# Kernel tuning notes

Measured on AMD Instinct MI355X. Metric: run time of the kernel, lower is better.

## Reference

```python
import jax, jax.numpy as jnp
import numpy as np

EPS = 1e-6
TOPK = 2
N_EXPERTS = 8


def setup_inputs() -> dict:
    key = jax.random.key(0)
    ks = jax.random.split(key, 6)
    B, S, H, I, E = 4, 2048, 2048, 1408, N_EXPERTS
    scale = 0.02
    return {
        "hidden_states": jax.random.normal(ks[0], (B, S, H), dtype=jnp.float32),
        "rms_weight": jnp.ones((H,), dtype=jnp.float32) + 0.01 * jax.random.normal(ks[1], (H,), dtype=jnp.float32),
        "router_weight": scale * jax.random.normal(ks[2], (E, H), dtype=jnp.float32),
        "w_gate": scale * jax.random.normal(ks[3], (E, I, H), dtype=jnp.float32),
        "w_up": scale * jax.random.normal(ks[4], (E, I, H), dtype=jnp.float32),
        "w_down": scale * jax.random.normal(ks[5], (E, H, I), dtype=jnp.float32),
    }


def reference(hidden_states, rms_weight, router_weight, w_gate, w_up, w_down):
    shape = hidden_states.shape
    H = shape[-1]
    x = hidden_states.reshape(-1, H).astype(jnp.float32)  # [T, H]

    # RMSNorm in fp32
    var = jnp.mean(x * x, axis=-1, keepdims=True)
    x = x * jax.lax.rsqrt(var + EPS) * rms_weight

    # Router (fp32 linear) + softmax over experts, then top-k of probs
    router_logits = x @ router_weight.T  # [T, E]
    probs = jax.nn.softmax(router_logits, axis=-1)
    topk_weight, indices = jax.lax.top_k(probs, TOPK)  # [T, k] sorted desc

    # normalize_top_k_affinities=True
    topk_weight = topk_weight / (jnp.sum(topk_weight, axis=-1, keepdims=True) + 1e-20)

    # Per-token per-expert combine weight: cw[t,e] = sum_k topk_weight[t,k] * [indices[t,k]==e]
    onehot = (indices[:, :, None] == jnp.arange(N_EXPERTS)[None, None, :])  # [T, k, E]
    cw = jnp.sum(topk_weight[:, :, None] * onehot.astype(topk_weight.dtype), axis=1)  # [T, E]

    # Dense per-expert GLU MLP, weighted accumulate (faithful to gather-MLP-scatter + einsum combine)
    out = jnp.zeros_like(x)
    for e in range(N_EXPERTS):
        g = x @ w_gate[e].T            # [T, I]
        u = x @ w_up[e].T              # [T, I]
        h = jax.nn.silu(g) * u         # GLU with silu act (scaling=1, bias=0)
        y = h @ w_down[e].T            # [T, H]
        out = out + cw[:, e:e + 1] * y

    return out.reshape(shape), router_logits.reshape(shape[:-1] + (N_EXPERTS,))
```

## Files before the change

kernel.cpp:

```cpp
#include <hip/hip_runtime.h>

#define T_TOK 8192
#define HDIM 2048
#define IDIM 1408
#define NEXP 8

#define BM 128
#define BN 128
#define BK 64
#define LDK 72

typedef short s16x8 __attribute__((ext_vector_type(8)));
typedef float f32x4 __attribute__((ext_vector_type(4)));
typedef unsigned short ushort_t;

__device__ __forceinline__ ushort_t f2bf(float f) {
  unsigned int u = __float_as_uint(f);
  unsigned int r = (u + 0x7fffu + ((u >> 16) & 1u)) >> 16;
  return (ushort_t)r;
}

__device__ __forceinline__ void gll16(const void* g, void* lds) {
  __builtin_amdgcn_global_load_lds(
      (const __attribute__((address_space(1))) unsigned int*)g,
      (__attribute__((address_space(3))) unsigned int*)lds, 16, 0, 0);
}

__global__ __launch_bounds__(256) void k_cast(const float* __restrict__ src,
                                              ushort_t* __restrict__ dst, int n8) {
  int i = blockIdx.x * blockDim.x + threadIdx.x;
  if (i < n8) {
    float4 f0 = ((const float4*)src)[(size_t)i * 2];
    float4 f1 = ((const float4*)src)[(size_t)i * 2 + 1];
    union { ushort_t us[8]; uint4 v; } p;
    p.us[0]=f2bf(f0.x); p.us[1]=f2bf(f0.y); p.us[2]=f2bf(f0.z); p.us[3]=f2bf(f0.w);
    p.us[4]=f2bf(f1.x); p.us[5]=f2bf(f1.y); p.us[6]=f2bf(f1.z); p.us[7]=f2bf(f1.w);
    ((uint4*)dst)[i] = p.v;
  }
}

__global__ __launch_bounds__(256) void k_rms_router(
    const float* __restrict__ x, const float* __restrict__ rmsw,
    const float* __restrict__ rw, ushort_t* __restrict__ xnorm,
    float* __restrict__ logits_out, int* __restrict__ counts,
    int* __restrict__ tokens, float* __restrict__ pairw)
{
  const int t = blockIdx.x;
  const int tid = threadIdx.x;
  const float* xr = x + (size_t)t * HDIM + tid * 8;
  float4 a = *(const float4*)xr;
  float4 b = *(const float4*)(xr + 4);
  float xi[8] = {a.x, a.y, a.z, a.w, b.x, b.y, b.z, b.w};
  float ss = 0.f;
  #pragma unroll
  for (int i = 0; i < 8; i++) ss += xi[i] * xi[i];
  #pragma unroll
  for (int o = 32; o > 0; o >>= 1) ss += __shfl_down(ss, o, 64);
  __shared__ float s_red[4];
  if ((tid & 63) == 0) s_red[tid >> 6] = ss;
  __syncthreads();
  float tot = s_red[0] + s_red[1] + s_red[2] + s_red[3];
  float rstd = rsqrtf(tot * (1.0f / HDIM) + 1e-6f);

  const float* wwp = rmsw + tid * 8;
  #pragma unroll
  for (int i = 0; i < 8; i++) xi[i] = xi[i] * rstd * wwp[i];

  union { ushort_t us[8]; uint4 v; } pk;
  #pragma unroll
  for (int i = 0; i < 8; i++) pk.us[i] = f2bf(xi[i]);
  *(uint4*)(xnorm + (size_t)t * HDIM + tid * 8) = pk.v;

  float lg[8];
  #pragma unroll
  for (int e = 0; e < 8; e++) {
    const float4* wr = (const float4*)(rw + e * HDIM + tid * 8);
    float4 w0 = wr[0], w1 = wr[1];
    lg[e] = xi[0]*w0.x + xi[1]*w0.y + xi[2]*w0.z + xi[3]*w0.w
          + xi[4]*w1.x + xi[5]*w1.y + xi[6]*w1.z + xi[7]*w1.w;
  }
  #pragma unroll
  for (int e = 0; e < 8; e++) {
    #pragma unroll
    for (int o = 32; o > 0; o >>= 1) lg[e] += __shfl_down(lg[e], o, 64);
  }
  __shared__ float s_lg[4][8];
  if ((tid & 63) == 0) {
    #pragma unroll
    for (int e = 0; e < 8; e++) s_lg[tid >> 6][e] = lg[e];
  }
  __syncthreads();
  __shared__ float s_fin[8];
  if (tid < 8) {
    float l = s_lg[0][tid] + s_lg[1][tid] + s_lg[2][tid] + s_lg[3][tid];
    logits_out[(size_t)t * NEXP + tid] = l;
    s_fin[tid] = l;
  }
  __syncthreads();
  if (tid == 0) {
    int i0 = 0;
    #pragma unroll
    for (int e = 1; e < 8; e++) if (s_fin[e] > s_fin[i0]) i0 = e;
    int i1 = (i0 == 0) ? 1 : 0;
    #pragma unroll
    for (int e = 0; e < 8; e++) if (e != i0 && s_fin[e] > s_fin[i1]) i1 = e;
    float p1 = __expf(s_fin[i1] - s_fin[i0]);
    float inv = 1.0f / (1.0f + p1);
    float w0 = inv, w1 = p1 * inv;
    int s0 = atomicAdd(&counts[i0], 1);
    tokens[i0 * T_TOK + s0] = t; pairw[i0 * T_TOK + s0] = w0;
    int s1 = atomicAdd(&counts[i1], 1);
    tokens[i1 * T_TOK + s1] = t; pairw[i1 * T_TOK + s1] = w1;
  }
}

__global__ void k_scan(const int* __restrict__ counts, int* __restrict__ basep) {
  if (threadIdx.x == 0) {
    int s = 0;
    for (int e = 0; e < NEXP; e++) { basep[e] = s; s += counts[e]; }
  }
}


__global__ __launch_bounds__(256, 3) void k_gateup_bf16(
    const ushort_t* __restrict__ xnorm, const ushort_t* __restrict__ wgb,
    const ushort_t* __restrict__ wub, const int* __restrict__ tokens,
    const int* __restrict__ counts, const int* __restrict__ basep,
    ushort_t* __restrict__ hbuf)
{
  const int e = blockIdx.z;
  const int cnt = counts[e];
  const int m0 = blockIdx.x * BM;
  if (m0 >= cnt) return;
  const int r0 = blockIdx.y * 64;
  const int tid = threadIdx.x;

  __shared__ ushort_t As[BM * BK];
  __shared__ ushort_t Bs[BN * BK];

  const int lane = tid & 63;
  const int w = tid >> 6;
  const int srow = lane >> 3;
  const int scol = ((lane & 7) ^ srow) * 8;

  const ushort_t* agp[4]; const ushort_t* bgp[4];
  #pragma unroll
  for (int i = 0; i < 4; i++) {
    const int rl = (w * 4 + i) * 8 + srow;
    const int slot = (m0 + rl < cnt) ? (m0 + rl) : (cnt - 1);
    const int tok = tokens[e * T_TOK + slot];
    agp[i] = xnorm + (size_t)tok * HDIM + scol;
    const int nrow = r0 + ((rl >> 5) << 4) + (rl & 15);
    const ushort_t* wsrc = ((rl >> 4) & 1) ? wub : wgb;
    bgp[i] = wsrc + ((size_t)e * IDIM + nrow) * HDIM + scol;
  }

  const int wm = (w & 1) * 64;
  const int wn = (w >> 1) * 64;
  const int fr = lane & 15;
  const int fq = lane >> 4;
  const int sx = fr & 7;

  f32x4 acc[4][4] = {};

  for (int k0 = 0; k0 < HDIM; k0 += BK) {
    #pragma unroll
    for (int i = 0; i < 4; i++) gll16(agp[i] + k0, &As[(w * 4 + i) * 512]);
    #pragma unroll
    for (int i = 0; i < 4; i++) gll16(bgp[i] + k0, &Bs[(w * 4 + i) * 512]);
    __syncthreads();
    #pragma unroll
    for (int kk = 0; kk < BK; kk += 32) {
      const int c0 = kk >> 3;
      s16x8 af[4], bf[4];
      #pragma unroll
      for (int mi = 0; mi < 4; mi++)
        af[mi] = *(const s16x8*)(&As[(wm + mi * 16 + fr) * BK + (((c0 + fq) ^ sx) << 3)]);
      #pragma unroll
      for (int ni = 0; ni < 4; ni++)
        bf[ni] = *(const s16x8*)(&Bs[(wn + ni * 16 + fr) * BK + (((c0 + fq) ^ sx) << 3)]);
      #pragma unroll
      for (int mi = 0; mi < 4; mi++) {
        #pragma unroll
        for (int ni = 0; ni < 4; ni++)
          acc[mi][ni] = __builtin_amdgcn_mfma_f32_16x16x32_bf16(af[mi], bf[ni], acc[mi][ni], 0, 0, 0);
      }
    }
    __syncthreads();
  }

  const int hb = basep[e];
  #pragma unroll
  for (int mi = 0; mi < 4; mi++) {
    #pragma unroll
    for (int reg = 0; reg < 4; reg++) {
      const int rl = wm + mi * 16 + fq * 4 + reg;
      if (m0 + rl < cnt) {
        ushort_t* hrow = hbuf + (size_t)(hb + m0 + rl) * IDIM + r0 + (wn >> 1);
        #pragma unroll
        for (int nj = 0; nj < 2; nj++) {
          float g = acc[mi][2 * nj][reg];
          float u = acc[mi][2 * nj + 1][reg];
          float hv = (g / (1.0f + __expf(-g))) * u;
          hrow[nj * 16 + fr] = f2bf(hv);
        }
      }
    }
  }
}

__global__ __launch_bounds__(256, 3) void k_down_bf16(
    const ushort_t* __restrict__ hbuf, const ushort_t* __restrict__ wdb,
    const int* __restrict__ tokens, const float* __restrict__ pairw,
    const int* __restrict__ counts, const int* __restrict__ basep,
    float* __restrict__ out)
{
  const int e = blockIdx.z;
  const int cnt = counts[e];
  const int m0 = blockIdx.x * BM;
  if (m0 >= cnt) return;
  const int n0 = blockIdx.y * BN;
  const int tid = threadIdx.x;
  const int hb = basep[e];

  __shared__ ushort_t As[BM * BK];
  __shared__ ushort_t Bs[BN * BK];

  const int lane = tid & 63;
  const int w = tid >> 6;
  const int srow = lane >> 3;
  const int scol = ((lane & 7) ^ srow) * 8;

  const ushort_t* agp[4]; const ushort_t* bgp[4];
  #pragma unroll
  for (int i = 0; i < 4; i++) {
    const int rl = (w * 4 + i) * 8 + srow;
    const int slot = (m0 + rl < cnt) ? (m0 + rl) : (cnt - 1);
    agp[i] = hbuf + (size_t)(hb + slot) * IDIM + scol;
    bgp[i] = wdb + ((size_t)e * HDIM + n0 + rl) * IDIM + scol;
  }

  const int wm = (w & 1) * 64;
  const int wn = (w >> 1) * 64;
  const int fr = lane & 15;
  const int fq = lane >> 4;
  const int sx = fr & 7;

  f32x4 acc[4][4] = {};

  for (int k0 = 0; k0 < IDIM; k0 += BK) {
    #pragma unroll
    for (int i = 0; i < 4; i++) gll16(agp[i] + k0, &As[(w * 4 + i) * 512]);
    #pragma unroll
    for (int i = 0; i < 4; i++) gll16(bgp[i] + k0, &Bs[(w * 4 + i) * 512]);
    __syncthreads();
    #pragma unroll
    for (int kk = 0; kk < BK; kk += 32) {
      const int c0 = kk >> 3;
      s16x8 af[4], bf[4];
      #pragma unroll
      for (int mi = 0; mi < 4; mi++)
        af[mi] = *(const s16x8*)(&As[(wm + mi * 16 + fr) * BK + (((c0 + fq) ^ sx) << 3)]);
      #pragma unroll
      for (int ni = 0; ni < 4; ni++)
        bf[ni] = *(const s16x8*)(&Bs[(wn + ni * 16 + fr) * BK + (((c0 + fq) ^ sx) << 3)]);
      #pragma unroll
      for (int mi = 0; mi < 4; mi++) {
        #pragma unroll
        for (int ni = 0; ni < 4; ni++)
          acc[mi][ni] = __builtin_amdgcn_mfma_f32_16x16x32_bf16(af[mi], bf[ni], acc[mi][ni], 0, 0, 0);
      }
    }
    __syncthreads();
  }

  #pragma unroll
  for (int mi = 0; mi < 4; mi++) {
    #pragma unroll
    for (int reg = 0; reg < 4; reg++) {
      const int rl = wm + mi * 16 + fq * 4 + reg;
      if (m0 + rl < cnt) {
        const int tok = tokens[e * T_TOK + m0 + rl];
        const float ww = pairw[e * T_TOK + m0 + rl];
        float* orow = out + (size_t)tok * HDIM + n0;
        #pragma unroll
        for (int ni = 0; ni < 4; ni++)
          atomicAdd(&orow[wn + ni * 16 + fr], ww * acc[mi][ni][reg]);
      }
    }
  }
}


__global__ __launch_bounds__(256, 2) void k_gateup_f32(
    const ushort_t* __restrict__ xnorm, const float* __restrict__ wg,
    const float* __restrict__ wu, const int* __restrict__ tokens,
    const int* __restrict__ counts, const int* __restrict__ basep,
    ushort_t* __restrict__ hbuf)
{
  const int e = blockIdx.z;
  const int cnt = counts[e];
  const int m0 = blockIdx.x * BM;
  if (m0 >= cnt) return;
  const int n0 = blockIdx.y * BN;
  const int tid = threadIdx.x;

  __shared__ ushort_t As[BM * LDK];
  __shared__ ushort_t Bgs[BN * LDK];
  __shared__ ushort_t Bus[BN * LDK];

  const int r = tid >> 1;
  const int col0 = (tid & 1) * 32;
  const int slot = (m0 + r < cnt) ? (m0 + r) : (cnt - 1);
  const int tok = tokens[e * T_TOK + slot];
  const ushort_t* asrc = xnorm + (size_t)tok * HDIM + col0;
  const float* gsrc = wg + ((size_t)e * IDIM + n0 + r) * HDIM + col0;
  const float* usrc = wu + ((size_t)e * IDIM + n0 + r) * HDIM + col0;

  const int lane = tid & 63;
  const int wid = tid >> 6;
  const int wm = (wid & 1) * 64;
  const int wn = (wid >> 1) * 64;
  const int fr = lane & 15;
  const int fq = lane >> 4;

  f32x4 accg[4][4] = {};
  f32x4 accu[4][4] = {};

  for (int k0 = 0; k0 < HDIM; k0 += BK) {
    #pragma unroll
    for (int i = 0; i < 4; i++) {
      uint4 v = *(const uint4*)(asrc + k0 + i * 8);
      *(uint4*)(&As[r * LDK + col0 + i * 8]) = v;
    }
    #pragma unroll
    for (int i = 0; i < 4; i++) {
      float4 f0 = *(const float4*)(gsrc + k0 + i * 8);
      float4 f1 = *(const float4*)(gsrc + k0 + i * 8 + 4);
      union { ushort_t us[8]; uint4 v; } p;
      p.us[0]=f2bf(f0.x); p.us[1]=f2bf(f0.y); p.us[2]=f2bf(f0.z); p.us[3]=f2bf(f0.w);
      p.us[4]=f2bf(f1.x); p.us[5]=f2bf(f1.y); p.us[6]=f2bf(f1.z); p.us[7]=f2bf(f1.w);
      *(uint4*)(&Bgs[r * LDK + col0 + i * 8]) = p.v;
    }
    #pragma unroll
    for (int i = 0; i < 4; i++) {
      float4 f0 = *(const float4*)(usrc + k0 + i * 8);
      float4 f1 = *(const float4*)(usrc + k0 + i * 8 + 4);
      union { ushort_t us[8]; uint4 v; } p;
      p.us[0]=f2bf(f0.x); p.us[1]=f2bf(f0.y); p.us[2]=f2bf(f0.z); p.us[3]=f2bf(f0.w);
      p.us[4]=f2bf(f1.x); p.us[5]=f2bf(f1.y); p.us[6]=f2bf(f1.z); p.us[7]=f2bf(f1.w);
      *(uint4*)(&Bus[r * LDK + col0 + i * 8]) = p.v;
    }
    __syncthreads();
    #pragma unroll
    for (int kk = 0; kk < BK; kk += 32) {
      s16x8 af[4], bg[4], bu[4];
      #pragma unroll
      for (int mi = 0; mi < 4; mi++)
        af[mi] = *(const s16x8*)(&As[(wm + mi * 16 + fr) * LDK + kk + fq * 8]);
      #pragma unroll
      for (int ni = 0; ni < 4; ni++) {
        bg[ni] = *(const s16x8*)(&Bgs[(wn + ni * 16 + fr) * LDK + kk + fq * 8]);
        bu[ni] = *(const s16x8*)(&Bus[(wn + ni * 16 + fr) * LDK + kk + fq * 8]);
      }
      #pragma unroll
      for (int mi = 0; mi < 4; mi++) {
        #pragma unroll
        for (int ni = 0; ni < 4; ni++) {
          accg[mi][ni] = __builtin_amdgcn_mfma_f32_16x16x32_bf16(af[mi], bg[ni], accg[mi][ni], 0, 0, 0);
          accu[mi][ni] = __builtin_amdgcn_mfma_f32_16x16x32_bf16(af[mi], bu[ni], accu[mi][ni], 0, 0, 0);
        }
      }
    }
    __syncthreads();
  }

  const int hb = basep[e];
  #pragma unroll
  for (int mi = 0; mi < 4; mi++) {
    #pragma unroll
    for (int reg = 0; reg < 4; reg++) {
      const int rl = wm + mi * 16 + fq * 4 + reg;
      if (m0 + rl < cnt) {
        ushort_t* hrow = hbuf + (size_t)(hb + m0 + rl) * IDIM + n0;
        #pragma unroll
        for (int ni = 0; ni < 4; ni++) {
          float g = accg[mi][ni][reg];
          float u = accu[mi][ni][reg];
          float hv = (g / (1.0f + __expf(-g))) * u;
          hrow[wn + ni * 16 + fr] = f2bf(hv);
        }
      }
    }
  }
}

__global__ __launch_bounds__(256, 2) void k_down_f32(
    const ushort_t* __restrict__ hbuf, const float* __restrict__ wd,
    const int* __restrict__ tokens, const float* __restrict__ pairw,
    const int* __restrict__ counts, const int* __restrict__ basep,
    float* __restrict__ out)
{
  const int e = blockIdx.z;
  const int cnt = counts[e];
  const int m0 = blockIdx.x * BM;
  if (m0 >= cnt) return;
  const int n0 = blockIdx.y * BN;
  const int tid = threadIdx.x;
  const int hb = basep[e];

  __shared__ ushort_t As[BM * LDK];
  __shared__ ushort_t Bs[BN * LDK];

  const int r = tid >> 1;
  const int col0 = (tid & 1) * 32;
  const int slot = (m0 + r < cnt) ? (m0 + r) : (cnt - 1);
  const ushort_t* asrc = hbuf + (size_t)(hb + slot) * IDIM + col0;
  const float* bsrc = wd + ((size_t)e * HDIM + n0 + r) * IDIM + col0;

  const int lane = tid & 63;
  const int wid = tid >> 6;
  const int wm = (wid & 1) * 64;
  const int wn = (wid >> 1) * 64;
  const int fr = lane & 15;
  const int fq = lane >> 4;

  f32x4 acc[4][4] = {};

  for (int k0 = 0; k0 < IDIM; k0 += BK) {
    #pragma unroll
    for (int i = 0; i < 4; i++) {
      uint4 v = *(const uint4*)(asrc + k0 + i * 8);
      *(uint4*)(&As[r * LDK + col0 + i * 8]) = v;
    }
    #pragma unroll
    for (int i = 0; i < 4; i++) {
      float4 f0 = *(const float4*)(bsrc + k0 + i * 8);
      float4 f1 = *(const float4*)(bsrc + k0 + i * 8 + 4);
      union { ushort_t us[8]; uint4 v; } p;
      p.us[0]=f2bf(f0.x); p.us[1]=f2bf(f0.y); p.us[2]=f2bf(f0.z); p.us[3]=f2bf(f0.w);
      p.us[4]=f2bf(f1.x); p.us[5]=f2bf(f1.y); p.us[6]=f2bf(f1.z); p.us[7]=f2bf(f1.w);
      *(uint4*)(&Bs[r * LDK + col0 + i * 8]) = p.v;
    }
    __syncthreads();
    #pragma unroll
    for (int kk = 0; kk < BK; kk += 32) {
      s16x8 af[4], bf[4];
      #pragma unroll
      for (int mi = 0; mi < 4; mi++)
        af[mi] = *(const s16x8*)(&As[(wm + mi * 16 + fr) * LDK + kk + fq * 8]);
      #pragma unroll
      for (int ni = 0; ni < 4; ni++)
        bf[ni] = *(const s16x8*)(&Bs[(wn + ni * 16 + fr) * LDK + kk + fq * 8]);
      #pragma unroll
      for (int mi = 0; mi < 4; mi++) {
        #pragma unroll
        for (int ni = 0; ni < 4; ni++)
          acc[mi][ni] = __builtin_amdgcn_mfma_f32_16x16x32_bf16(af[mi], bf[ni], acc[mi][ni], 0, 0, 0);
      }
    }
    __syncthreads();
  }

  #pragma unroll
  for (int mi = 0; mi < 4; mi++) {
    #pragma unroll
    for (int reg = 0; reg < 4; reg++) {
      const int rl = wm + mi * 16 + fq * 4 + reg;
      if (m0 + rl < cnt) {
        const int tok = tokens[e * T_TOK + m0 + rl];
        const float ww = pairw[e * T_TOK + m0 + rl];
        float* orow = out + (size_t)tok * HDIM + n0;
        #pragma unroll
        for (int ni = 0; ni < 4; ni++)
          atomicAdd(&orow[wn + ni * 16 + fr], ww * acc[mi][ni][reg]);
      }
    }
  }
}

extern "C" void kernel_launch(void* const* d_in, const int* in_sizes, int n_in,
                              void* d_out, int out_size, void* d_ws, size_t ws_size,
                              hipStream_t stream)
{
  (void)in_sizes; (void)n_in;
  const float* x    = (const float*)d_in[0];
  const float* rmsw = (const float*)d_in[1];
  const float* rw   = (const float*)d_in[2];
  const float* wg   = (const float*)d_in[3];
  const float* wu   = (const float*)d_in[4];
  const float* wd   = (const float*)d_in[5];
  float* out = (float*)d_out;
  float* logits_out = out + (size_t)T_TOK * HDIM;

  const size_t WB = (size_t)NEXP * IDIM * HDIM * 2;
  const size_t HB = (size_t)2 * T_TOK * IDIM * 2;
  const size_t XB = (size_t)T_TOK * HDIM * 2;
  const size_t BOOK = 1024 + 2 * (size_t)NEXP * T_TOK * 4;

  char* ws = (char*)d_ws;
  int* counts  = (int*)ws;
  int* basep   = (int*)(ws + 256);
  int* tokens  = (int*)(ws + 1024);
  float* pairw = (float*)(ws + 1024 + (size_t)NEXP * T_TOK * 4);

  hipMemsetAsync(d_out, 0, (size_t)out_size * sizeof(float), stream);
  hipMemsetAsync(d_ws, 0, 512, stream);

  const size_t NEED = BOOK + HB + 2 * WB + ((WB > XB) ? WB : XB) + 4096;
  const int n8 = (int)((size_t)NEXP * IDIM * HDIM / 8);

  if (ws_size >= NEED) {
    ushort_t* hbuf  = (ushort_t*)(ws + BOOK);
    ushort_t* wgb   = (ushort_t*)(ws + BOOK + HB);
    ushort_t* wub   = (ushort_t*)(ws + BOOK + HB + WB);
    ushort_t* xnorm = (ushort_t*)(ws + BOOK + HB + 2 * WB);
    ushort_t* wdb   = (ushort_t*)(ws + BOOK + HB + 2 * WB);

    k_cast<<<(n8 + 255) / 256, 256, 0, stream>>>(wg, wgb, n8);
    k_cast<<<(n8 + 255) / 256, 256, 0, stream>>>(wu, wub, n8);
    k_rms_router<<<T_TOK, 256, 0, stream>>>(x, rmsw, rw, xnorm, logits_out,
                                            counts, tokens, pairw);
    k_scan<<<1, 64, 0, stream>>>(counts, basep);
    k_gateup_bf16<<<dim3(T_TOK / BM, IDIM / 64, NEXP), 256, 0, stream>>>(
        xnorm, wgb, wub, tokens, counts, basep, hbuf);
    k_cast<<<(n8 + 255) / 256, 256, 0, stream>>>(wd, wdb, n8);
    k_down_bf16<<<dim3(T_TOK / BM, HDIM / BN, NEXP), 256, 0, stream>>>(
        hbuf, wdb, tokens, pairw, counts, basep, out);
  } else {
    ushort_t* xnorm = (ushort_t*)(ws + BOOK);
    ushort_t* hbuf  = (ushort_t*)(ws + BOOK + XB);

    k_rms_router<<<T_TOK, 256, 0, stream>>>(x, rmsw, rw, xnorm, logits_out,
                                            counts, tokens, pairw);
    k_scan<<<1, 64, 0, stream>>>(counts, basep);
    k_gateup_f32<<<dim3(T_TOK / BM, IDIM / BN, NEXP), 256, 0, stream>>>(
        xnorm, wg, wu, tokens, counts, basep, hbuf);
    k_down_f32<<<dim3(T_TOK / BM, HDIM / BN, NEXP), 256, 0, stream>>>(
        hbuf, wd, tokens, pairw, counts, basep, out);
  }
}
```

Baseline: 1.077 ms.

## Rewrite bf16 expert GEMMs as 256x256 tiles with double-buffered async LDS pipeline

The bf16 gate/up and down GEMM kernels move to 512-thread blocks computing 256x256 tiles. Global-to-LDS loads are split into k-halves, double-buffered and prefetched one to two tiles ahead, with explicit vmcnt/lgkmcnt waits, raw barriers and setprio around the MFMA bursts. The aim is to hide load latency behind matrix math and to raise arithmetic intensity per loaded byte. The costs are 64KB of LDS per block, more accumulator registers, lower occupancy, and more wasted work on partial expert tiles because M-tiles are now twice as large.

```diff
diff --git a/kernel.cpp b/kernel.cpp
--- a/kernel.cpp
+++ b/kernel.cpp
@@ -5,10 +5,8 @@
 #define IDIM 1408
 #define NEXP 8
 
-#define BM 128
-#define BN 128
-#define BK 64
 #define LDK 72
+#define BKF 64
 
 typedef short s16x8 __attribute__((ext_vector_type(8)));
 typedef float f32x4 __attribute__((ext_vector_type(4)));
@@ -122,7 +120,43 @@
 }
 
 
-__global__ __launch_bounds__(256, 3) void k_gateup_bf16(
+#define GEMM_PHASE(PAR, KH, H, READB, STAGE_STMT, TAIL_STMT)                         \
+  {                                                                                  \
+    s16x8 af[4];                                                                     \
+    _Pragma("unroll") for (int j = 0; j < 4; j++) {                                  \
+      const int r_ = wr * 128 + ((H) * 4 + j) * 16 + fr;                             \
+      af[j] = *(const s16x8*)&sA[PAR][KH][(size_t)r_ * 32 + ((fq ^ (r_ & 3)) << 3)]; \
+    }                                                                                \
+    if (READB) {                                                                     \
+      _Pragma("unroll") for (int n = 0; n < 4; n++) {                                \
+        const int r_ = wc * 64 + n * 16 + fr;                                        \
+        bfr[n] = *(const s16x8*)&sB[PAR][KH][(size_t)r_ * 32 + ((fq ^ (r_ & 3)) << 3)]; \
+      }                                                                              \
+    }                                                                                \
+    STAGE_STMT;                                                                      \
+    __builtin_amdgcn_s_barrier();                                                    \
+    asm volatile("s_waitcnt lgkmcnt(0)" ::: "memory");                               \
+    __builtin_amdgcn_sched_barrier(0);                                               \
+    __builtin_amdgcn_s_setprio(1);                                                   \
+    _Pragma("unroll") for (int j = 0; j < 4; j++)                                    \
+      _Pragma("unroll") for (int n = 0; n < 4; n++)                                  \
+        acc[(H) * 4 + j][n] = __builtin_amdgcn_mfma_f32_16x16x32_bf16(               \
+            af[j], bfr[n], acc[(H) * 4 + j][n], 0, 0, 0);                            \
+    __builtin_amdgcn_s_setprio(0);                                                   \
+    TAIL_STMT;                                                                       \
+    __builtin_amdgcn_s_barrier();                                                    \
+  }
+
+#define STAGE_A(P, KH, T) do {                                                       \
+    gll16(aB0 + (size_t)((T) * 64 + (KH) * 32), &sA[P][KH][w * 512]);                \
+    gll16(aB1 + (size_t)((T) * 64 + (KH) * 32), &sA[P][KH][4096 + w * 512]); } while (0)
+#define STAGE_B(P, KH, T) do {                                                       \
+    gll16(bB0 + (size_t)((T) * 64 + (KH) * 32), &sB[P][KH][w * 512]);                \
+    gll16(bB1 + (size_t)((T) * 64 + (KH) * 32), &sB[P][KH][4096 + w * 512]); } while (0)
+
+#define VMW8 asm volatile("s_waitcnt vmcnt(8)" ::: "memory")
+
+__global__ __launch_bounds__(512) void k_gateup_bf16(
     const ushort_t* __restrict__ xnorm, const ushort_t* __restrict__ wgb,
     const ushort_t* __restrict__ wub, const int* __restrict__ tokens,
     const int* __restrict__ counts, const int* __restrict__ basep,
@@ -130,86 +164,73 @@
 {
   const int e = blockIdx.z;
   const int cnt = counts[e];
-  const int m0 = blockIdx.x * BM;
+  const int m0 = blockIdx.x * 256;
   if (m0 >= cnt) return;
-  const int r0 = blockIdx.y * 64;
+  const int r0 = blockIdx.y * 128;
   const int tid = threadIdx.x;
-
-  __shared__ ushort_t As[BM * BK];
-  __shared__ ushort_t Bs[BN * BK];
-
   const int lane = tid & 63;
   const int w = tid >> 6;
-  const int srow = lane >> 3;
-  const int scol = ((lane & 7) ^ srow) * 8;
-
-  const ushort_t* agp[4]; const ushort_t* bgp[4];
-  #pragma unroll
-  for (int i = 0; i < 4; i++) {
-    const int rl = (w * 4 + i) * 8 + srow;
-    const int slot = (m0 + rl < cnt) ? (m0 + rl) : (cnt - 1);
-    const int tok = tokens[e * T_TOK + slot];
-    agp[i] = xnorm + (size_t)tok * HDIM + scol;
-    const int nrow = r0 + ((rl >> 5) << 4) + (rl & 15);
-    const ushort_t* wsrc = ((rl >> 4) & 1) ? wub : wgb;
-    bgp[i] = wsrc + ((size_t)e * IDIM + nrow) * HDIM + scol;
-  }
-
-  const int wm = (w & 1) * 64;
-  const int wn = (w >> 1) * 64;
-  const int fr = lane & 15;
-  const int fq = lane >> 4;
-  const int sx = fr & 7;
-
-  f32x4 acc[4][4] = {};
-
-  for (int k0 = 0; k0 < HDIM; k0 += BK) {
-    #pragma unroll
-    for (int i = 0; i < 4; i++) gll16(agp[i] + k0, &As[(w * 4 + i) * 512]);
-    #pragma unroll
-    for (int i = 0; i < 4; i++) gll16(bgp[i] + k0, &Bs[(w * 4 + i) * 512]);
-    __syncthreads();
-    #pragma unroll
-    for (int kk = 0; kk < BK; kk += 32) {
-      const int c0 = kk >> 3;
-      s16x8 af[4], bf[4];
-      #pragma unroll
-      for (int mi = 0; mi < 4; mi++)
-        af[mi] = *(const s16x8*)(&As[(wm + mi * 16 + fr) * BK + (((c0 + fq) ^ sx) << 3)]);
-      #pragma unroll
-      for (int ni = 0; ni < 4; ni++)
-        bf[ni] = *(const s16x8*)(&Bs[(wn + ni * 16 + fr) * BK + (((c0 + fq) ^ sx) << 3)]);
-      #pragma unroll
-      for (int mi = 0; mi < 4; mi++) {
-        #pragma unroll
-        for (int ni = 0; ni < 4; ni++)
-          acc[mi][ni] = __builtin_amdgcn_mfma_f32_16x16x32_bf16(af[mi], bf[ni], acc[mi][ni], 0, 0, 0);
-      }
-    }
-    __syncthreads();
+  const int wr = w >> 2, wc = w & 3;
+  const int fr = lane & 15, fq = lane >> 4;
+
+  __shared__ ushort_t sA[2][2][8192];
+  __shared__ ushort_t sB[2][2][8192];
+
+  const int srow = w * 16 + (lane >> 2);
+  const int sch  = ((lane & 3) ^ ((lane >> 2) & 3)) * 8;
+
+  const ushort_t *aB0, *aB1, *bB0, *bB1;
+  {
+    int rl = srow;
+    int slot = (m0 + rl < cnt) ? m0 + rl : cnt - 1;
+    aB0 = xnorm + (size_t)tokens[e * T_TOK + slot] * HDIM + sch;
+    int nrow = r0 + ((rl >> 5) << 4) + (rl & 15);
+    bB0 = (((rl >> 4) & 1) ? wub : wgb) + ((size_t)e * IDIM + nrow) * HDIM + sch;
+    rl = 128 + srow;
+    slot = (m0 + rl < cnt) ? m0 + rl : cnt - 1;
+    aB1 = xnorm + (size_t)tokens[e * T_TOK + slot] * HDIM + sch;
+    nrow = r0 + ((rl >> 5) << 4) + (rl & 15);
+    bB1 = (((rl >> 4) & 1) ? wub : wgb) + ((size_t)e * IDIM + nrow) * HDIM + sch;
+  }
+
+  f32x4 acc[8][4] = {};
+  const int NT = HDIM / 64;
+
+  STAGE_A(0, 0, 0); STAGE_B(0, 0, 0); STAGE_A(0, 1, 0); STAGE_B(0, 1, 0);
+  STAGE_A(1, 0, 1); STAGE_B(1, 0, 1);
+  asm volatile("s_waitcnt vmcnt(4)" ::: "memory");
+  __builtin_amdgcn_s_barrier();
+
+  for (int kt = 0; kt < NT; ++kt) {
+    const int par = kt & 1, nxt = par ^ 1;
+    s16x8 bfr[4];
+    GEMM_PHASE(par, 0, 0, 1, if (kt + 1 < NT) STAGE_A(nxt, 1, kt + 1), );
+    GEMM_PHASE(par, 0, 1, 0, if (kt + 1 < NT) STAGE_B(nxt, 1, kt + 1), VMW8);
+    GEMM_PHASE(par, 1, 0, 1, if (kt + 2 < NT) STAGE_A(par, 0, kt + 2), );
+    GEMM_PHASE(par, 1, 1, 0, if (kt + 2 < NT) STAGE_B(par, 0, kt + 2), VMW8);
   }
 
   const int hb = basep[e];
   #pragma unroll
-  for (int mi = 0; mi < 4; mi++) {
+  for (int mi = 0; mi < 8; mi++) {
     #pragma unroll
     for (int reg = 0; reg < 4; reg++) {
-      const int rl = wm + mi * 16 + fq * 4 + reg;
+      const int rl = wr * 128 + mi * 16 + fq * 4 + reg;
       if (m0 + rl < cnt) {
-        ushort_t* hrow = hbuf + (size_t)(hb + m0 + rl) * IDIM + r0 + (wn >> 1);
+        ushort_t* hrow = hbuf + (size_t)(hb + m0 + rl) * IDIM + r0;
         #pragma unroll
         for (int nj = 0; nj < 2; nj++) {
           float g = acc[mi][2 * nj][reg];
           float u = acc[mi][2 * nj + 1][reg];
           float hv = (g / (1.0f + __expf(-g))) * u;
-          hrow[nj * 16 + fr] = f2bf(hv);
+          hrow[(wc * 2 + nj) * 16 + fr] = f2bf(hv);
         }
       }
     }
   }
 }
 
-__global__ __launch_bounds__(256, 3) void k_down_bf16(
+__global__ __launch_bounds__(512) void k_down_bf16(
     const ushort_t* __restrict__ hbuf, const ushort_t* __restrict__ wdb,
     const int* __restrict__ tokens, const float* __restrict__ pairw,
     const int* __restrict__ counts, const int* __restrict__ basep,
@@ -217,75 +238,63 @@
 {
   const int e = blockIdx.z;
   const int cnt = counts[e];
-  const int m0 = blockIdx.x * BM;
+  const int m0 = blockIdx.x * 256;
   if (m0 >= cnt) return;
-  const int n0 = blockIdx.y * BN;
+  const int n0 = blockIdx.y * 256;
   const int tid = threadIdx.x;
   const int hb = basep[e];
-
-  __shared__ ushort_t As[BM * BK];
-  __shared__ ushort_t Bs[BN * BK];
-
   const int lane = tid & 63;
   const int w = tid >> 6;
-  const int srow = lane >> 3;
-  const int scol = ((lane & 7) ^ srow) * 8;
-
-  const ushort_t* agp[4]; const ushort_t* bgp[4];
-  #pragma unroll
-  for (int i = 0; i < 4; i++) {
-    const int rl = (w * 4 + i) * 8 + srow;
-    const int slot = (m0 + rl < cnt) ? (m0 + rl) : (cnt - 1);
-    agp[i] = hbuf + (size_t)(hb + slot) * IDIM + scol;
-    bgp[i] = wdb + ((size_t)e * HDIM + n0 + rl) * IDIM + scol;
-  }
-
-  const int wm = (w & 1) * 64;
-  const int wn = (w >> 1) * 64;
-  const int fr = lane & 15;
-  const int fq = lane >> 4;
-  const int sx = fr & 7;
-
-  f32x4 acc[4][4] = {};
-
-  for (int k0 = 0; k0 < IDIM; k0 += BK) {
-    #pragma unroll
-    for (int i = 0; i < 4; i++) gll16(agp[i] + k0, &As[(w * 4 + i) * 512]);
-    #pragma unroll
-    for (int i = 0; i < 4; i++) gll16(bgp[i] + k0, &Bs[(w * 4 + i) * 512]);
-    __syncthreads();
-    #pragma unroll
-    for (int kk = 0; kk < BK; kk += 32) {
-      const int c0 = kk >> 3;
-      s16x8 af[4], bf[4];
-      #pragma unroll
-      for (int mi = 0; mi < 4; mi++)
-        af[mi] = *(const s16x8*)(&As[(wm + mi * 16 + fr) * BK + (((c0 + fq) ^ sx) << 3)]);
-      #pragma unroll
-      for (int ni = 0; ni < 4; ni++)
-        bf[ni] = *(const s16x8*)(&Bs[(wn + ni * 16 + fr) * BK + (((c0 + fq) ^ sx) << 3)]);
-      #pragma unroll
-      for (int mi = 0; mi < 4; mi++) {
-        #pragma unroll
-        for (int ni = 0; ni < 4; ni++)
-          acc[mi][ni] = __builtin_amdgcn_mfma_f32_16x16x32_bf16(af[mi], bf[ni], acc[mi][ni], 0, 0, 0);
-      }
-    }
-    __syncthreads();
-  }
-
-  #pragma unroll
-  for (int mi = 0; mi < 4; mi++) {
+  const int wr = w >> 2, wc = w & 3;
+  const int fr = lane & 15, fq = lane >> 4;
+
+  __shared__ ushort_t sA[2][2][8192];
+  __shared__ ushort_t sB[2][2][8192];
+
+  const int srow = w * 16 + (lane >> 2);
+  const int sch  = ((lane & 3) ^ ((lane >> 2) & 3)) * 8;
+
+  const ushort_t *aB0, *aB1, *bB0, *bB1;
+  {
+    int rl = srow;
+    int slot = (m0 + rl < cnt) ? m0 + rl : cnt - 1;
+    aB0 = hbuf + (size_t)(hb + slot) * IDIM + sch;
+    bB0 = wdb + ((size_t)e * HDIM + n0 + rl) * IDIM + sch;
+    rl = 128 + srow;
+    slot = (m0 + rl < cnt) ? m0 + rl : cnt - 1;
+    aB1 = hbuf + (size_t)(hb + slot) * IDIM + sch;
+    bB1 = wdb + ((size_t)e * HDIM + n0 + rl) * IDIM + sch;
+  }
+
+  f32x4 acc[8][4] = {};
+  const int NT = IDIM / 64;
+
+  STAGE_A(0, 0, 0); STAGE_B(0, 0, 0); STAGE_A(0, 1, 0); STAGE_B(0, 1, 0);
+  STAGE_A(1, 0, 1); STAGE_B(1, 0, 1);
+  asm volatile("s_waitcnt vmcnt(4)" ::: "memory");
+  __builtin_amdgcn_s_barrier();
+
+  for (int kt = 0; kt < NT; ++kt) {
+    const int par = kt & 1, nxt = par ^ 1;
+    s16x8 bfr[4];
+    GEMM_PHASE(par, 0, 0, 1, if (kt + 1 < NT) STAGE_A(nxt, 1, kt + 1), );
+    GEMM_PHASE(par, 0, 1, 0, if (kt + 1 < NT) STAGE_B(nxt, 1, kt + 1), VMW8);
+    GEMM_PHASE(par, 1, 0, 1, if (kt + 2 < NT) STAGE_A(par, 0, kt + 2), );
+    GEMM_PHASE(par, 1, 1, 0, if (kt + 2 < NT) STAGE_B(par, 0, kt + 2), VMW8);
+  }
+
+  #pragma unroll
+  for (int mi = 0; mi < 8; mi++) {
     #pragma unroll
     for (int reg = 0; reg < 4; reg++) {
-      const int rl = wm + mi * 16 + fq * 4 + reg;
+      const int rl = wr * 128 + mi * 16 + fq * 4 + reg;
       if (m0 + rl < cnt) {
         const int tok = tokens[e * T_TOK + m0 + rl];
         const float ww = pairw[e * T_TOK + m0 + rl];
         float* orow = out + (size_t)tok * HDIM + n0;
         #pragma unroll
         for (int ni = 0; ni < 4; ni++)
-          atomicAdd(&orow[wn + ni * 16 + fr], ww * acc[mi][ni][reg]);
+          atomicAdd(&orow[wc * 64 + ni * 16 + fr], ww * acc[mi][ni][reg]);
       }
     }
   }
@@ -300,14 +309,14 @@
 {
   const int e = blockIdx.z;
   const int cnt = counts[e];
-  const int m0 = blockIdx.x * BM;
+  const int m0 = blockIdx.x * 128;
   if (m0 >= cnt) return;
-  const int n0 = blockIdx.y * BN;
+  const int n0 = blockIdx.y * 128;
   const int tid = threadIdx.x;
 
-  __shared__ ushort_t As[BM * LDK];
-  __shared__ ushort_t Bgs[BN * LDK];
-  __shared__ ushort_t Bus[BN * LDK];
+  __shared__ ushort_t As[128 * LDK];
+  __shared__ ushort_t Bgs[128 * LDK];
+  __shared__ ushort_t Bus[128 * LDK];
 
   const int r = tid >> 1;
   const int col0 = (tid & 1) * 32;
@@ -327,7 +336,7 @@
   f32x4 accg[4][4] = {};
   f32x4 accu[4][4] = {};
 
-  for (int k0 = 0; k0 < HDIM; k0 += BK) {
+  for (int k0 = 0; k0 < HDIM; k0 += BKF) {
     #pragma unroll
     for (int i = 0; i < 4; i++) {
       uint4 v = *(const uint4*)(asrc + k0 + i * 8);
@@ -353,7 +362,7 @@
     }
     __syncthreads();
     #pragma unroll
-    for (int kk = 0; kk < BK; kk += 32) {
+    for (int kk = 0; kk < BKF; kk += 32) {
       s16x8 af[4], bg[4], bu[4];
       #pragma unroll
       for (int mi = 0; mi < 4; mi++)
@@ -403,14 +412,14 @@
 {
   const int e = blockIdx.z;
   const int cnt = counts[e];
-  const int m0 = blockIdx.x * BM;
+  const int m0 = blockIdx.x * 128;
   if (m0 >= cnt) return;
-  const int n0 = blockIdx.y * BN;
+  const int n0 = blockIdx.y * 128;
   const int tid = threadIdx.x;
   const int hb = basep[e];
 
-  __shared__ ushort_t As[BM * LDK];
-  __shared__ ushort_t Bs[BN * LDK];
+  __shared__ ushort_t As[128 * LDK];
+  __shared__ ushort_t Bs[128 * LDK];
 
   const int r = tid >> 1;
   const int col0 = (tid & 1) * 32;
@@ -427,7 +436,7 @@
 
   f32x4 acc[4][4] = {};
 
-  for (int k0 = 0; k0 < IDIM; k0 += BK) {
+  for (int k0 = 0; k0 < IDIM; k0 += BKF) {
     #pragma unroll
     for (int i = 0; i < 4; i++) {
       uint4 v = *(const uint4*)(asrc + k0 + i * 8);
@@ -444,7 +453,7 @@
     }
     __syncthreads();
     #pragma unroll
-    for (int kk = 0; kk < BK; kk += 32) {
+    for (int kk = 0; kk < BKF; kk += 32) {
       s16x8 af[4], bf[4];
       #pragma unroll
       for (int mi = 0; mi < 4; mi++)
@@ -522,10 +531,10 @@
     k_rms_router<<<T_TOK, 256, 0, stream>>>(x, rmsw, rw, xnorm, logits_out,
                                             counts, tokens, pairw);
     k_scan<<<1, 64, 0, stream>>>(counts, basep);
-    k_gateup_bf16<<<dim3(T_TOK / BM, IDIM / 64, NEXP), 256, 0, stream>>>(
+    k_gateup_bf16<<<dim3(T_TOK / 256, (2 * IDIM) / 256, NEXP), 512, 0, stream>>>(
         xnorm, wgb, wub, tokens, counts, basep, hbuf);
     k_cast<<<(n8 + 255) / 256, 256, 0, stream>>>(wd, wdb, n8);
-    k_down_bf16<<<dim3(T_TOK / BM, HDIM / BN, NEXP), 256, 0, stream>>>(
+    k_down_bf16<<<dim3(T_TOK / 256, HDIM / 256, NEXP), 512, 0, stream>>>(
         hbuf, wdb, tokens, pairw, counts, basep, out);
   } else {
     ushort_t* xnorm = (ushort_t*)(ws + BOOK);
@@ -534,9 +543,9 @@
     k_rms_router<<<T_TOK, 256, 0, stream>>>(x, rmsw, rw, xnorm, logits_out,
                                             counts, tokens, pairw);
     k_scan<<<1, 64, 0, stream>>>(counts, basep);
-    k_gateup_f32<<<dim3(T_TOK / BM, IDIM / BN, NEXP), 256, 0, stream>>>(
+    k_gateup_f32<<<dim3(T_TOK / 128, IDIM / 128, NEXP), 256, 0, stream>>>(
         xnorm, wg, wu, tokens, counts, basep, hbuf);
-    k_down_f32<<<dim3(T_TOK / BM, HDIM / BN, NEXP), 256, 0, stream>>>(
+    k_down_f32<<<dim3(T_TOK / 128, HDIM / 128, NEXP), 256, 0, stream>>>(
         hbuf, wd, tokens, pairw, counts, basep, out);
   }
 }
```

Result: slower. 2.009 ms (+86.6%).

## Compact expert tile list, XCD-aware block remap, replace atomics with two-buffer combine

Applied to the files above, without the earlier changes.

Builds a compact list of (expert, m-tile) work items in the scan kernel so the grouped GEMMs launch only real tiles instead of a sparse 3D grid with early exits. Block IDs are remapped so that consecutive tiles land on the same XCD, which is meant to improve L2 reuse of weights. The down projection now writes plain stores into one of two output buffers chosen by top-k rank, and a combine kernel adds them, removing the memset and the float atomics. Occupancy hints are raised to 4 blocks per CU. The cost is an extra full-output read/write pass and a workspace buffer that reuses the gate/up weight region.

```diff
diff --git a/kernel.cpp b/kernel.cpp
--- a/kernel.cpp
+++ b/kernel.cpp
@@ -8,6 +8,7 @@
 #define BM 128
 #define BN 128
 #define BK 64
+#define NTILE_MAX 136
 #define LDK 72
 
 typedef short s16x8 __attribute__((ext_vector_type(8)));
@@ -24,6 +25,12 @@
   __builtin_amdgcn_global_load_lds(
       (const __attribute__((address_space(1))) unsigned int*)g,
       (__attribute__((address_space(3))) unsigned int*)lds, 16, 0, 0);
+}
+
+__device__ __forceinline__ int xcd_remap(int orig, int nwg) {
+  const int q = nwg >> 3, r = nwg & 7;
+  const int x = orig & 7, i = orig >> 3;
+  return (x < r ? x * (q + 1) : r * (q + 1) + (x - r) * q) + i;
 }
 
 __global__ __launch_bounds__(256) void k_cast(const float* __restrict__ src,
@@ -43,7 +50,8 @@
     const float* __restrict__ x, const float* __restrict__ rmsw,
     const float* __restrict__ rw, ushort_t* __restrict__ xnorm,
     float* __restrict__ logits_out, int* __restrict__ counts,
-    int* __restrict__ tokens, float* __restrict__ pairw)
+    int* __restrict__ tokens, float* __restrict__ pairw,
+    int* __restrict__ ranks)
 {
   const int t = blockIdx.x;
   const int tid = threadIdx.x;
@@ -108,31 +116,44 @@
     float inv = 1.0f / (1.0f + p1);
     float w0 = inv, w1 = p1 * inv;
     int s0 = atomicAdd(&counts[i0], 1);
-    tokens[i0 * T_TOK + s0] = t; pairw[i0 * T_TOK + s0] = w0;
+    tokens[i0 * T_TOK + s0] = t; pairw[i0 * T_TOK + s0] = w0; ranks[i0 * T_TOK + s0] = 0;
     int s1 = atomicAdd(&counts[i1], 1);
-    tokens[i1 * T_TOK + s1] = t; pairw[i1 * T_TOK + s1] = w1;
-  }
-}
-
-__global__ void k_scan(const int* __restrict__ counts, int* __restrict__ basep) {
+    tokens[i1 * T_TOK + s1] = t; pairw[i1 * T_TOK + s1] = w1; ranks[i1 * T_TOK + s1] = 1;
+  }
+}
+
+__global__ void k_scan(const int* __restrict__ counts, int* __restrict__ basep,
+                       int* __restrict__ tile_e, int* __restrict__ tile_m,
+                       int* __restrict__ ntile) {
   if (threadIdx.x == 0) {
-    int s = 0;
-    for (int e = 0; e < NEXP; e++) { basep[e] = s; s += counts[e]; }
-  }
-}
-
-
-__global__ __launch_bounds__(256, 3) void k_gateup_bf16(
+    int s = 0, nt = 0;
+    for (int e = 0; e < NEXP; e++) {
+      basep[e] = s;
+      for (int m0 = 0; m0 < counts[e]; m0 += BM) { tile_e[nt] = e; tile_m[nt] = m0; nt++; }
+      s += counts[e];
+    }
+    *ntile = nt;
+  }
+}
+
+
+__global__ __launch_bounds__(256, 4) void k_gateup_bf16(
     const ushort_t* __restrict__ xnorm, const ushort_t* __restrict__ wgb,
     const ushort_t* __restrict__ wub, const int* __restrict__ tokens,
     const int* __restrict__ counts, const int* __restrict__ basep,
-    ushort_t* __restrict__ hbuf)
+    const int* __restrict__ tile_e, const int* __restrict__ tile_m,
+    const int* __restrict__ ntile, ushort_t* __restrict__ hbuf)
 {
-  const int e = blockIdx.z;
+  const int nwg = gridDim.x * gridDim.y;
+  int flat = blockIdx.x + gridDim.x * blockIdx.y;
+  flat = xcd_remap(flat, nwg);
+  const int bx = flat % gridDim.x;
+  const int by = flat / gridDim.x;
+  if (bx >= *ntile) return;
+  const int e = tile_e[bx];
+  const int m0 = tile_m[bx];
   const int cnt = counts[e];
-  const int m0 = blockIdx.x * BM;
-  if (m0 >= cnt) return;
-  const int r0 = blockIdx.y * 64;
+  const int r0 = by * 64;
   const int tid = threadIdx.x;
 
   __shared__ ushort_t As[BM * BK];
@@ -209,17 +230,24 @@
   }
 }
 
-__global__ __launch_bounds__(256, 3) void k_down_bf16(
+__global__ __launch_bounds__(256, 4) void k_down_bf16(
     const ushort_t* __restrict__ hbuf, const ushort_t* __restrict__ wdb,
     const int* __restrict__ tokens, const float* __restrict__ pairw,
-    const int* __restrict__ counts, const int* __restrict__ basep,
-    float* __restrict__ out)
+    const int* __restrict__ ranks, const int* __restrict__ counts,
+    const int* __restrict__ basep, const int* __restrict__ tile_e,
+    const int* __restrict__ tile_m, const int* __restrict__ ntile,
+    float* __restrict__ out, float* __restrict__ out_b)
 {
-  const int e = blockIdx.z;
+  const int nwg = gridDim.x * gridDim.y;
+  int flat = blockIdx.x + gridDim.x * blockIdx.y;
+  flat = xcd_remap(flat, nwg);
+  const int bx = flat % gridDim.x;
+  const int by = flat / gridDim.x;
+  if (bx >= *ntile) return;
+  const int e = tile_e[bx];
+  const int m0 = tile_m[bx];
   const int cnt = counts[e];
-  const int m0 = blockIdx.x * BM;
-  if (m0 >= cnt) return;
-  const int n0 = blockIdx.y * BN;
+  const int n0 = by * BN;
   const int tid = threadIdx.x;
   const int hb = basep[e];
 
@@ -280,14 +308,28 @@
     for (int reg = 0; reg < 4; reg++) {
       const int rl = wm + mi * 16 + fq * 4 + reg;
       if (m0 + rl < cnt) {
-        const int tok = tokens[e * T_TOK + m0 + rl];
-        const float ww = pairw[e * T_TOK + m0 + rl];
-        float* orow = out + (size_t)tok * HDIM + n0;
+        const int idx = e * T_TOK + m0 + rl;
+        const int tok = tokens[idx];
+        const float ww = pairw[idx];
+        float* obase = ranks[idx] ? out_b : out;
+        float* orow = obase + (size_t)tok * HDIM + n0;
         #pragma unroll
         for (int ni = 0; ni < 4; ni++)
-          atomicAdd(&orow[wn + ni * 16 + fr], ww * acc[mi][ni][reg]);
-      }
-    }
+          orow[wn + ni * 16 + fr] = ww * acc[mi][ni][reg];
+      }
+    }
+  }
+}
+
+__global__ __launch_bounds__(256) void k_combine(float* __restrict__ out,
+                                                 const float* __restrict__ outb, int n4) {
+  int i = blockIdx.x * blockDim.x + threadIdx.x;
+  const int stride = gridDim.x * blockDim.x;
+  for (; i < n4; i += stride) {
+    float4 a = ((const float4*)out)[i];
+    float4 b = ((const float4*)outb)[i];
+    a.x += b.x; a.y += b.y; a.z += b.z; a.w += b.w;
+    ((float4*)out)[i] = a;
   }
 }
 
@@ -496,15 +538,18 @@
   const size_t WB = (size_t)NEXP * IDIM * HDIM * 2;
   const size_t HB = (size_t)2 * T_TOK * IDIM * 2;
   const size_t XB = (size_t)T_TOK * HDIM * 2;
-  const size_t BOOK = 1024 + 2 * (size_t)NEXP * T_TOK * 4;
+  const size_t BOOK = 2048 + 3 * (size_t)NEXP * T_TOK * 4;
 
   char* ws = (char*)d_ws;
   int* counts  = (int*)ws;
   int* basep   = (int*)(ws + 256);
-  int* tokens  = (int*)(ws + 1024);
-  float* pairw = (float*)(ws + 1024 + (size_t)NEXP * T_TOK * 4);
-
-  hipMemsetAsync(d_out, 0, (size_t)out_size * sizeof(float), stream);
+  int* ntile   = (int*)(ws + 320);
+  int* tile_e  = (int*)(ws + 384);
+  int* tile_m  = (int*)(ws + 1024);
+  int* tokens  = (int*)(ws + 2048);
+  float* pairw = (float*)(ws + 2048 + (size_t)NEXP * T_TOK * 4);
+  int* ranks   = (int*)(ws + 2048 + 2 * (size_t)NEXP * T_TOK * 4);
+
   hipMemsetAsync(d_ws, 0, 512, stream);
 
   const size_t NEED = BOOK + HB + 2 * WB + ((WB > XB) ? WB : XB) + 4096;
@@ -516,24 +561,28 @@
     ushort_t* wub   = (ushort_t*)(ws + BOOK + HB + WB);
     ushort_t* xnorm = (ushort_t*)(ws + BOOK + HB + 2 * WB);
     ushort_t* wdb   = (ushort_t*)(ws + BOOK + HB + 2 * WB);
+    float* out_b    = (float*)(ws + BOOK + HB);
 
     k_cast<<<(n8 + 255) / 256, 256, 0, stream>>>(wg, wgb, n8);
     k_cast<<<(n8 + 255) / 256, 256, 0, stream>>>(wu, wub, n8);
     k_rms_router<<<T_TOK, 256, 0, stream>>>(x, rmsw, rw, xnorm, logits_out,
-                                            counts, tokens, pairw);
-    k_scan<<<1, 64, 0, stream>>>(counts, basep);
-    k_gateup_bf16<<<dim3(T_TOK / BM, IDIM / 64, NEXP), 256, 0, stream>>>(
-        xnorm, wgb, wub, tokens, counts, basep, hbuf);
+                                            counts, tokens, pairw, ranks);
+    k_scan<<<1, 64, 0, stream>>>(counts, basep, tile_e, tile_m, ntile);
+    k_gateup_bf16<<<dim3(NTILE_MAX, IDIM / 64), 256, 0, stream>>>(
+        xnorm, wgb, wub, tokens, counts, basep, tile_e, tile_m, ntile, hbuf);
     k_cast<<<(n8 + 255) / 256, 256, 0, stream>>>(wd, wdb, n8);
-    k_down_bf16<<<dim3(T_TOK / BM, HDIM / BN, NEXP), 256, 0, stream>>>(
-        hbuf, wdb, tokens, pairw, counts, basep, out);
+    k_down_bf16<<<dim3(NTILE_MAX, HDIM / BN), 256, 0, stream>>>(
+        hbuf, wdb, tokens, pairw, ranks, counts, basep, tile_e, tile_m, ntile,
+        out, out_b);
+    k_combine<<<2048, 256, 0, stream>>>(out, out_b, (int)((size_t)T_TOK * HDIM / 4));
   } else {
     ushort_t* xnorm = (ushort_t*)(ws + BOOK);
     ushort_t* hbuf  = (ushort_t*)(ws + BOOK + XB);
 
+    hipMemsetAsync(d_out, 0, (size_t)out_size * sizeof(float), stream);
     k_rms_router<<<T_TOK, 256, 0, stream>>>(x, rmsw, rw, xnorm, logits_out,
-                                            counts, tokens, pairw);
-    k_scan<<<1, 64, 0, stream>>>(counts, basep);
+                                            counts, tokens, pairw, ranks);
+    k_scan<<<1, 64, 0, stream>>>(counts, basep, tile_e, tile_m, ntile);
     k_gateup_f32<<<dim3(T_TOK / BM, IDIM / BN, NEXP), 256, 0, stream>>>(
         xnorm, wg, wu, tokens, counts, basep, hbuf);
     k_down_f32<<<dim3(T_TOK / BM, HDIM / BN, NEXP), 256, 0, stream>>>(
```

New measurement: 1.233 ms. 1.14x slower.
